# Performance work log

Hardware: AMD Instinct MI355X
Metric: run time of the kernel (lower is better)

Reference implementation:

```python
import jax, jax.numpy as jnp
import numpy as np

EPS_AGG = 1e-6
EPS_BN = 1e-5
EPS_LN = 1e-5


def _bn(t, g, b):
    # BatchNorm1d in training mode: batch statistics over dim 0
    m = t.mean(0)
    v = t.var(0)
    return (t - m) * jax.lax.rsqrt(v + EPS_BN) * g + b


def _gated_gcn(x, e, src, dst, Aw, Ab, Bw, Bb, Cw, Cb, Dw, Db, Ew, Eb, gx, bx, ge, be):
    # GraphGPS GatedGCNLayer (residual=True, dropout=0, no PE)
    N = x.shape[0]
    Ax = x @ Aw + Ab
    Bx = x @ Bw + Bb
    Ce = e @ Cw + Cb
    Dx = x @ Dw + Db
    Ex = x @ Ew + Eb
    e_new = Dx[dst] + Ex[src] + Ce            # [E, D] edge gates (i=target, j=source)
    sig = jax.nn.sigmoid(e_new)
    num = jax.ops.segment_sum(sig * Bx[src], dst, num_segments=N)
    den = jax.ops.segment_sum(sig, dst, num_segments=N) + EPS_AGG
    x_new = Ax + num / den
    x = x + jax.nn.relu(_bn(x_new, gx, bx))   # BN -> ReLU -> residual
    e = e + jax.nn.relu(_bn(e_new, ge, be))
    return x, e


def setup_inputs() -> dict:
    key = jax.random.key(0)
    G, NPG, DEG, D = 256, 32, 8, 70
    NC, H = 10, 256
    N, E = G * NPG, G * NPG * DEG
    ks = list(jax.random.split(key, 24))

    def nrm(k, shape):
        return jax.random.normal(k, shape, jnp.float32)

    def lin(k, i, o):
        return nrm(k, (i, o)) / np.float32(np.sqrt(i)), jnp.zeros((o,), jnp.float32)

    x = nrm(ks[0], (N, 1))
    edge_attr = nrm(ks[1], (E, 1))
    base = jnp.repeat(jnp.arange(G, dtype=jnp.int32) * NPG, NPG * DEG)
    src = base + jax.random.randint(ks[2], (E,), 0, NPG, dtype=jnp.int32)
    dst = base + jax.random.randint(ks[3], (E,), 0, NPG, dtype=jnp.int32)
    edge_index = jnp.stack([src, dst])
    batch_index = jnp.repeat(jnp.arange(G, dtype=jnp.int32), NPG)

    inp = {"x": x, "edge_index": edge_index, "edge_attr": edge_attr, "batch_index": batch_index}
    inp["w_node"], inp["b_node"] = lin(ks[4], 1, D)
    inp["w_edge"], inp["b_edge"] = lin(ks[5], 1, D)
    i = 6
    for l in ("1", "2"):
        for nm in ("A", "B", "C", "D", "E"):
            inp[nm + l + "w"], inp[nm + l + "b"] = lin(ks[i], D, D)
            i += 1
        inp["gx" + l], inp["bx" + l] = jnp.ones((D,), jnp.float32), jnp.zeros((D,), jnp.float32)
        inp["ge" + l], inp["be" + l] = jnp.ones((D,), jnp.float32), jnp.zeros((D,), jnp.float32)
    inp["cls1_w"], inp["cls1_b"] = lin(ks[i], 2 * D, H)
    i += 1
    inp["ln_g"], inp["ln_b"] = jnp.ones((H,), jnp.float32), jnp.zeros((H,), jnp.float32)
    inp["cls2_w"], inp["cls2_b"] = lin(ks[i], H, NC)
    return inp


def reference(x, edge_index, edge_attr, batch_index,
              w_node, b_node, w_edge, b_edge,
              A1w, A1b, B1w, B1b, C1w, C1b, D1w, D1b, E1w, E1b, gx1, bx1, ge1, be1,
              A2w, A2b, B2w, B2b, C2w, C2b, D2w, D2b, E2w, E2b, gx2, bx2, ge2, be2,
              cls1_w, cls1_b, ln_g, ln_b, cls2_w, cls2_b):
    src, dst = edge_index[0], edge_index[1]
    bi = np.asarray(batch_index)
    n_iters = int(np.bincount(bi).max() // 2)   # int(max(sizes)/2)
    B = int(bi.max()) + 1

    h = x @ w_node + b_node
    e = edge_attr @ w_edge + b_edge
    h, e = _gated_gcn(h, e, src, dst, A1w, A1b, B1w, B1b, C1w, C1b, D1w, D1b, E1w, E1b, gx1, bx1, ge1, be1)
    for _ in range(n_iters):  # shared conv2 weights
        h, e = _gated_gcn(h, e, src, dst, A2w, A2b, B2w, B2b, C2w, C2b, D2w, D2b, E2w, E2b, gx2, bx2, ge2, be2)

    gmp = jax.ops.segment_max(h, batch_index, num_segments=B)
    cnt = jax.ops.segment_sum(jnp.ones((h.shape[0], 1), h.dtype), batch_index, num_segments=B)
    gap = jax.ops.segment_sum(h, batch_index, num_segments=B) / cnt
    g = jnp.concatenate([gmp, gap], axis=1)            # [B, 2*D]
    g = jax.nn.relu(g @ cls1_w + cls1_b)               # [B, 256]
    mu = g.mean(-1, keepdims=True)
    var = g.var(-1, keepdims=True)
    g = (g - mu) * jax.lax.rsqrt(var + EPS_LN) * ln_g + ln_b
    return g @ cls2_w + cls2_b                         # [B, num_classes]
```

## Files before the change

kernel.cpp:

```cpp
#include <hip/hip_runtime.h>
#include <hip/hip_fp16.h>
#include <math.h>


#define TPB 768
#define NBLK 256
#define DD 70
#define ETS 256
#define NBS 84
#define WTS 80
#define NLAYERS 17
#define SPL 280
#define NSLOT 8
#define EPS_AGG 1e-6f
#define EPS_BN 1e-5f
#define EPS_LN 1e-5f

#define SCX 0
#define SHX 72
#define SCE 144
#define SHE 216
#define SBO 288
#define STATL_F 576

#define OFF_ET   0
#define OFF_HN   (OFF_ET + 72*ETS)
#define OFF_AX   (OFF_HN + 32*NBS)
#define OFF_BX   (OFF_AX + 32*NBS)
#define OFF_DX   (OFF_BX + 32*NBS)
#define OFF_EX   (OFF_DX + 32*NBS)
#define OFF_PAD  (OFF_EX + 32*NBS)
#define OFF_STATL (OFF_PAD + 3584)
#define SMEM_FLOATS (OFF_STATL + STATL_F)
#define SMEM_BYTES  (SMEM_FLOATS*4 + (32+33)*4 + 512 + 512 + 16)

#define EIX(k,e) (((k)<<8) + ((e) ^ ((((k)>>2)&7)<<2)))
#define SIX(j,c) (((j)<<7) + ((c) ^ ((j)&30)))

#define WS_STATS 4096
#define WS_WT    163840

struct GPSParams {
  const float* __restrict__ x; const int* __restrict__ ei; const float* __restrict__ ea;
  const float* __restrict__ wn; const float* __restrict__ bnn;
  const float* __restrict__ we; const float* __restrict__ web;
  const float* __restrict__ Aw[2]; const float* __restrict__ Ab[2];
  const float* __restrict__ Bw[2]; const float* __restrict__ Bb[2];
  const float* __restrict__ Cw[2]; const float* __restrict__ Cb[2];
  const float* __restrict__ Dw[2]; const float* __restrict__ Db[2];
  const float* __restrict__ Ew[2]; const float* __restrict__ Eb[2];
  const float* __restrict__ gx[2]; const float* __restrict__ bx[2];
  const float* __restrict__ ge[2]; const float* __restrict__ gbe[2];
  const float* __restrict__ c1w; const float* __restrict__ c1b;
  const float* __restrict__ lng; const float* __restrict__ lnb;
  const float* __restrict__ c2w; const float* __restrict__ c2b;
  float* __restrict__ out; float* __restrict__ stats; float* __restrict__ wt;
  unsigned* __restrict__ bar;
};

__device__ __forceinline__ void grid_sync(unsigned* b) {
  __syncthreads();
  if (threadIdx.x == 0) {
    unsigned g = __hip_atomic_load(b, __ATOMIC_RELAXED, __HIP_MEMORY_SCOPE_AGENT);
    int leaf = (int)(blockIdx.x >> 4);
    unsigned a = __hip_atomic_fetch_add(b + 32 + leaf*32, 1u, __ATOMIC_ACQ_REL, __HIP_MEMORY_SCOPE_AGENT);
    bool done = false;
    if (a == 15u) {
      unsigned r = __hip_atomic_fetch_add(b + 16, 1u, __ATOMIC_ACQ_REL, __HIP_MEMORY_SCOPE_AGENT);
      if (r == 15u) {
        #pragma unroll
        for (int i2 = 0; i2 < 16; ++i2)
          __hip_atomic_store(b + 32 + i2*32, 0u, __ATOMIC_RELAXED, __HIP_MEMORY_SCOPE_AGENT);
        __hip_atomic_store(b + 16, 0u, __ATOMIC_RELAXED, __HIP_MEMORY_SCOPE_AGENT);
        __hip_atomic_store(b, g + 1u, __ATOMIC_RELEASE, __HIP_MEMORY_SCOPE_AGENT);
        done = true;
      }
    }
    if (!done) {
      while (__hip_atomic_load(b, __ATOMIC_ACQUIRE, __HIP_MEMORY_SCOPE_AGENT) == g)
        __builtin_amdgcn_s_sleep(2);
    }
  }
  __syncthreads();
}

__global__ void __launch_bounds__(TPB)
__attribute__((amdgpu_waves_per_eu(3, 3)))
gps_kernel(GPSParams p) {
  extern __shared__ float smem[];
  float* eT    = smem + OFF_ET;
  float* hN    = smem + OFF_HN;
  float* Ax    = smem + OFF_AX;
  float* Bx    = smem + OFF_BX;
  float* Dx    = smem + OFF_DX;
  float* Ex    = smem + OFF_EX;
  float* statl = smem + OFF_STATL;
  unsigned* sigb = (unsigned*)(smem + OFF_DX);
  const __half* sigh = (const __half*)sigb;
  int*   icur  = (int*)(smem + SMEM_FLOATS);
  int*   ioff  = icur + 32;
  unsigned char* srcloc = (unsigned char*)(ioff + 33);
  unsigned char* dstloc = srcloc + 256;
  unsigned short* eidxS = (unsigned short*)(dstloc + 256);

  const int tid  = threadIdx.x;
  const int g    = blockIdx.x;
  const int lane = tid & 63;
  const int wid  = tid >> 6;

  const int jbe = wid * 6;
  const int e0  = lane * 4;
  const int n_m  = wid & 3;
  const int n_jb = (wid >> 2) * 24 + (lane >> 3) * 3;
  const int n_n0 = (lane & 7) * 4;

  float* slot = p.stats + ((g & 7) * NLAYERS) * SPL;

  if (tid < 32) icur[tid] = 0;
  __syncthreads();
  if (tid < 256) {
    int s0 = p.ei[g*256 + tid]         - g*32;
    int d0 = p.ei[65536 + g*256 + tid] - g*32;
    srcloc[tid] = (unsigned char)s0;
    dstloc[tid] = (unsigned char)d0;
    atomicAdd(&icur[d0], 1);
  }
  __syncthreads();
  if (tid == 0) {
    int o = 0;
    for (int n = 0; n < 32; ++n) { ioff[n] = o; o += icur[n]; }
    ioff[32] = o;
  }
  __syncthreads();
  if (tid < 32) icur[tid] = ioff[tid];
  __syncthreads();
  if (tid < 256) {
    int d0 = dstloc[tid];
    int sl2 = atomicAdd(&icur[d0], 1);
    eidxS[sl2] = (unsigned short)(tid | ((int)srcloc[tid] << 8));
  }

  for (int i = tid; i < SMEM_FLOATS - OFF_HN; i += TPB) smem[OFF_HN + i] = 0.f;
  for (int i = tid; i < 2*ETS; i += TPB) eT[70*ETS + i] = 0.f;
  __syncthreads();
  for (int i = tid; i < 32*DD; i += TPB) {
    int n = i / DD, j = i % DD;
    hN[n*NBS + j] = fmaf(p.x[g*32 + n], p.wn[j], p.bnn[j]);
  }
  for (int i = tid; i < DD*256; i += TPB) {
    int k = i >> 8, e = i & 255;
    eT[EIX(k, e)] = fmaf(p.ea[g*256 + e], p.we[k], p.web[k]);
  }

  if (g < 10) {
    int ss = g / 5, mm = g % 5;
    const float* W = (mm==0) ? p.Aw[ss] : (mm==1) ? p.Bw[ss] : (mm==2) ? p.Cw[ss]
                   : (mm==3) ? p.Dw[ss] : p.Ew[ss];
    float* dst = p.wt + g * (72*WTS);
    for (int i = tid; i < 72*WTS; i += TPB) {
      int j = i / WTS, k = i - j*WTS;
      dst[i] = (j < DD && k < DD) ? W[k*DD + j] : 0.f;
    }
  }
  grid_sync(p.bar);

  #pragma unroll 1
  for (int L = 0; L < NLAYERS; ++L) {
    const int s = (L == 0) ? 0 : 1;
    float* lslot = slot + L * SPL;
    const float* wbase = p.wt + (size_t)(s*5) * (72*WTS);

    if (tid < DD) statl[SBO + tid] = p.Cb[s][tid] + p.Db[s][tid] + p.Eb[s][tid];

    {
      const float* Wm = wbase + ((n_m==0) ? 0 : (n_m==1) ? 1 : (n_m==2) ? 3 : 4) * (72*WTS);
      float* nbuf = (n_m==0) ? Ax : (n_m==1) ? Bx : (n_m==2) ? Dx : Ex;
      const float* nbias = (n_m==1) ? p.Bb[s] : p.Ab[s];
      float acc[3][4];
      #pragma unroll
      for (int i = 0; i < 3; ++i)
        #pragma unroll
        for (int n = 0; n < 4; ++n) acc[i][n] = 0.f;
      const float* hr0 = hN + n_n0*NBS;
      #pragma unroll 2
      for (int c = 0; c < 18; ++c) {
        const int k0 = c*4;
        float4 h0 = *(const float4*)(hr0 + 0*NBS + k0);
        float4 h1 = *(const float4*)(hr0 + 1*NBS + k0);
        float4 h2 = *(const float4*)(hr0 + 2*NBS + k0);
        float4 h3 = *(const float4*)(hr0 + 3*NBS + k0);
        #pragma unroll
        for (int i = 0; i < 3; ++i) {
          float4 w4 = *(const float4*)(Wm + (n_jb + i)*WTS + k0);
          acc[i][0] = fmaf(h0.x, w4.x, acc[i][0]); acc[i][0] = fmaf(h0.y, w4.y, acc[i][0]);
          acc[i][0] = fmaf(h0.z, w4.z, acc[i][0]); acc[i][0] = fmaf(h0.w, w4.w, acc[i][0]);
          acc[i][1] = fmaf(h1.x, w4.x, acc[i][1]); acc[i][1] = fmaf(h1.y, w4.y, acc[i][1]);
          acc[i][1] = fmaf(h1.z, w4.z, acc[i][1]); acc[i][1] = fmaf(h1.w, w4.w, acc[i][1]);
          acc[i][2] = fmaf(h2.x, w4.x, acc[i][2]); acc[i][2] = fmaf(h2.y, w4.y, acc[i][2]);
          acc[i][2] = fmaf(h2.z, w4.z, acc[i][2]); acc[i][2] = fmaf(h2.w, w4.w, acc[i][2]);
          acc[i][3] = fmaf(h3.x, w4.x, acc[i][3]); acc[i][3] = fmaf(h3.y, w4.y, acc[i][3]);
          acc[i][3] = fmaf(h3.z, w4.z, acc[i][3]); acc[i][3] = fmaf(h3.w, w4.w, acc[i][3]);
        }
      }
      #pragma unroll
      for (int i = 0; i < 3; ++i) {
        int j = n_jb + i;
        if (j < DD) {
          float b = (n_m < 2) ? nbias[j] : 0.f;
          #pragma unroll
          for (int n = 0; n < 4; ++n)
            nbuf[(n_n0 + n)*NBS + j] = acc[i][n] + b;
        }
      }
    }
    __syncthreads();

    const float* wC = wbase + 2 * (72*WTS);
    float eacc[4][6];
    #pragma unroll
    for (int r = 0; r < 4; ++r)
      #pragma unroll
      for (int i = 0; i < 6; ++i) eacc[r][i] = 0.f;

    #pragma unroll 2
    for (int c = 0; c < 18; ++c) {
      const int k0 = c*4;
      float4 ev0 = *(const float4*)(eT + EIX(k0+0, e0));
      float4 ev1 = *(const float4*)(eT + EIX(k0+1, e0));
      float4 ev2 = *(const float4*)(eT + EIX(k0+2, e0));
      float4 ev3 = *(const float4*)(eT + EIX(k0+3, e0));
      #pragma unroll
      for (int i = 0; i < 6; ++i) {
        float4 w4 = *(const float4*)(wC + (jbe + i)*WTS + k0);
        eacc[0][i] = fmaf(ev0.x, w4.x, eacc[0][i]); eacc[1][i] = fmaf(ev0.y, w4.x, eacc[1][i]);
        eacc[2][i] = fmaf(ev0.z, w4.x, eacc[2][i]); eacc[3][i] = fmaf(ev0.w, w4.x, eacc[3][i]);
        eacc[0][i] = fmaf(ev1.x, w4.y, eacc[0][i]); eacc[1][i] = fmaf(ev1.y, w4.y, eacc[1][i]);
        eacc[2][i] = fmaf(ev1.z, w4.y, eacc[2][i]); eacc[3][i] = fmaf(ev1.w, w4.y, eacc[3][i]);
        eacc[0][i] = fmaf(ev2.x, w4.z, eacc[0][i]); eacc[1][i] = fmaf(ev2.y, w4.z, eacc[1][i]);
        eacc[2][i] = fmaf(ev2.z, w4.z, eacc[2][i]); eacc[3][i] = fmaf(ev2.w, w4.z, eacc[3][i]);
        eacc[0][i] = fmaf(ev3.x, w4.w, eacc[0][i]); eacc[1][i] = fmaf(ev3.y, w4.w, eacc[1][i]);
        eacc[2][i] = fmaf(ev3.z, w4.w, eacc[2][i]); eacc[3][i] = fmaf(ev3.w, w4.w, eacc[3][i]);
      }
    }

    {
      int dl0 = dstloc[e0],   sl0 = srcloc[e0];
      int dl1 = dstloc[e0+1], sl1 = srcloc[e0+1];
      int dl2 = dstloc[e0+2], sl2 = srcloc[e0+2];
      int dl3 = dstloc[e0+3], sl3 = srcloc[e0+3];
      #pragma unroll
      for (int i = 0; i < 6; ++i) {
        int j = jbe + i;
        if (j < DD) {
          float bb = statl[SBO + j];
          eacc[0][i] += Dx[dl0*NBS + j] + Ex[sl0*NBS + j] + bb;
          eacc[1][i] += Dx[dl1*NBS + j] + Ex[sl1*NBS + j] + bb;
          eacc[2][i] += Dx[dl2*NBS + j] + Ex[sl2*NBS + j] + bb;
          eacc[3][i] += Dx[dl3*NBS + j] + Ex[sl3*NBS + j] + bb;
        }
      }
    }

    #pragma unroll
    for (int i = 0; i < 6; ++i) {
      int j = jbe + i;
      float ps = (eacc[0][i] + eacc[1][i]) + (eacc[2][i] + eacc[3][i]);
      float qs = eacc[0][i]*eacc[0][i];
      qs = fmaf(eacc[1][i], eacc[1][i], qs);
      qs = fmaf(eacc[2][i], eacc[2][i], qs);
      qs = fmaf(eacc[3][i], eacc[3][i], qs);
      #pragma unroll
      for (int d = 1; d < 64; d <<= 1) {
        ps += __shfl_xor(ps, d, 64);
        qs += __shfl_xor(qs, d, 64);
      }
      if (lane == 0 && j < DD) {
        atomicAdd(lslot + 140 + j, ps);
        atomicAdd(lslot + 210 + j, qs);
      }
    }
    __syncthreads();

    #pragma unroll
    for (int i = 0; i < 6; ++i) {
      int j = jbe + i;
      if (j < DD) {
        float s0 = 1.f / (1.f + __expf(-eacc[0][i]));
        float s1 = 1.f / (1.f + __expf(-eacc[1][i]));
        float s2 = 1.f / (1.f + __expf(-eacc[2][i]));
        float s3 = 1.f / (1.f + __expf(-eacc[3][i]));
        __half2 h01 = __floats2half2_rn(s0, s1);
        __half2 h23 = __floats2half2_rn(s2, s3);
        uint2 pk;
        pk.x = *reinterpret_cast<unsigned*>(&h01);
        pk.y = *reinterpret_cast<unsigned*>(&h23);
        *reinterpret_cast<uint2*>(sigb + SIX(j, 2*lane)) = pk;
      }
    }
    __syncthreads();

    if (tid < 576) {
      int n = tid / 18, jq = tid % 18;
      int j0 = jq * 4;
      bool v2 = (j0 + 2) < DD, v3 = (j0 + 3) < DD;
      float nm0 = 0.f, nm1 = 0.f, nm2 = 0.f, nm3 = 0.f;
      float dn0 = 0.f, dn1 = 0.f, dn2 = 0.f, dn3 = 0.f;
      int pb = ioff[n], pe = ioff[n + 1];
      for (int pp = pb; pp < pe; ++pp) {
        unsigned v = eidxS[pp];
        int e2 = v & 255, sl2 = v >> 8;
        int cb = e2 >> 1, h2 = e2 & 1;
        float s0 = __half2float(sigh[(SIX(j0+0, cb) << 1) + h2]);
        float s1 = __half2float(sigh[(SIX(j0+1, cb) << 1) + h2]);
        float s2 = v2 ? __half2float(sigh[(SIX(j0+2, cb) << 1) + h2]) : 0.f;
        float s3 = v3 ? __half2float(sigh[(SIX(j0+3, cb) << 1) + h2]) : 0.f;
        float4 b4 = *(const float4*)(Bx + sl2*NBS + j0);
        nm0 = fmaf(s0, b4.x, nm0); nm1 = fmaf(s1, b4.y, nm1);
        nm2 = fmaf(s2, b4.z, nm2); nm3 = fmaf(s3, b4.w, nm3);
        dn0 += s0; dn1 += s1; dn2 += s2; dn3 += s3;
      }
      float* axp = Ax + n*NBS + j0;
      float4 ax = *(const float4*)axp;
      ax.x += nm0 / (dn0 + EPS_AGG);
      ax.y += nm1 / (dn1 + EPS_AGG);
      ax.z += nm2 / (dn2 + EPS_AGG);
      ax.w += nm3 / (dn3 + EPS_AGG);
      *(float4*)axp = ax;
    }
    __syncthreads();

    if (tid < SPL) {
      int col = tid % DD, q = tid / DD;
      float sm = 0.f, sq = 0.f;
      #pragma unroll
      for (int r = 0; r < 8; ++r) {
        float v = Ax[(q*8 + r)*NBS + col];
        sm += v; sq = fmaf(v, v, sq);
      }
      atomicAdd(lslot + col, sm);
      atomicAdd(lslot + 70 + col, sq);
    }

    grid_sync(p.bar);

    if (tid < DD) {
      float sm = 0.f, sq = 0.f;
      #pragma unroll
      for (int sl2 = 0; sl2 < NSLOT; ++sl2) {
        const float* st = p.stats + (sl2*NLAYERS + L)*SPL;
        sm += __hip_atomic_load(st + tid,      __ATOMIC_RELAXED, __HIP_MEMORY_SCOPE_AGENT);
        sq += __hip_atomic_load(st + 70 + tid, __ATOMIC_RELAXED, __HIP_MEMORY_SCOPE_AGENT);
      }
      float mean = sm * (1.f/8192.f);
      float var  = sq * (1.f/8192.f) - mean*mean;
      float sc = p.gx[s][tid] * rsqrtf(var + EPS_BN);
      statl[SCX + tid] = sc;
      statl[SHX + tid] = fmaf(-mean, sc, p.bx[s][tid]);
    } else if (tid < 140) {
      int j = tid - DD;
      float sm = 0.f, sq = 0.f;
      #pragma unroll
      for (int sl2 = 0; sl2 < NSLOT; ++sl2) {
        const float* st = p.stats + (sl2*NLAYERS + L)*SPL;
        sm += __hip_atomic_load(st + 140 + j, __ATOMIC_RELAXED, __HIP_MEMORY_SCOPE_AGENT);
        sq += __hip_atomic_load(st + 210 + j, __ATOMIC_RELAXED, __HIP_MEMORY_SCOPE_AGENT);
      }
      float mean = sm * (1.f/65536.f);
      float var  = sq * (1.f/65536.f) - mean*mean;
      float sc = p.ge[s][j] * rsqrtf(var + EPS_BN);
      statl[SCE + j] = sc;
      statl[SHE + j] = fmaf(-mean, sc, p.gbe[s][j]);
    }
    __syncthreads();

    #pragma unroll
    for (int r = 0; r < 3; ++r) {
      int idx = tid + r*TPB;
      int n = idx / 72, j = idx - n*72;
      if (j < DD) {
        float xn = Ax[n*NBS + j];
        hN[n*NBS + j] += fmaxf(fmaf(xn, statl[SCX + j], statl[SHX + j]), 0.f);
      }
    }
    #pragma unroll
    for (int i = 0; i < 6; ++i) {
      int j = jbe + i;
      if (j < DD) {
        float sc = statl[SCE + j], sh = statl[SHE + j];
        float* ep = eT + EIX(j, e0);
        float4 eo = *(const float4*)ep;
        eo.x += fmaxf(fmaf(eacc[0][i], sc, sh), 0.f);
        eo.y += fmaxf(fmaf(eacc[1][i], sc, sh), 0.f);
        eo.z += fmaxf(fmaf(eacc[2][i], sc, sh), 0.f);
        eo.w += fmaxf(fmaf(eacc[3][i], sc, sh), 0.f);
        *(float4*)ep = eo;
      }
    }
    __syncthreads();
  }

  if (tid < DD) {
    float mx = -3.4e38f, sm = 0.f;
    #pragma unroll 4
    for (int r = 0; r < 32; ++r) {
      float v = hN[r*NBS + tid];
      mx = fmaxf(mx, v); sm += v;
    }
    statl[tid]      = mx;
    statl[70 + tid] = sm * (1.f/32.f);
  }
  __syncthreads();
  if (tid < 256) {
    float a = p.c1b[tid];
    for (int k = 0; k < DD; ++k) a = fmaf(statl[k],      p.c1w[k*256 + tid], a);
    for (int k = 0; k < DD; ++k) a = fmaf(statl[70 + k], p.c1w[(DD + k)*256 + tid], a);
    Ax[tid] = fmaxf(a, 0.f);
  }
  __syncthreads();
  if (tid == 0) {
    float sm = 0.f, sq = 0.f;
    for (int k = 0; k < 256; ++k) { float v = Ax[k]; sm += v; sq = fmaf(v, v, sq); }
    float mean = sm * (1.f/256.f);
    float var  = sq * (1.f/256.f) - mean*mean;
    statl[560] = mean;
    statl[561] = rsqrtf(var + EPS_LN);
  }
  __syncthreads();
  if (tid < 256) {
    float v = (Ax[tid] - statl[560]) * statl[561];
    Bx[tid] = fmaf(v, p.lng[tid], p.lnb[tid]);
  }
  __syncthreads();
  if (tid < 10) {
    float a = p.c2b[tid];
    for (int k = 0; k < 256; ++k) a = fmaf(Bx[k], p.c2w[k*10 + tid], a);
    p.out[g*10 + tid] = a;
  }
}

extern "C" void kernel_launch(void* const* d_in, const int* in_sizes, int n_in,
                              void* d_out, int out_size, void* d_ws, size_t ws_size,
                              hipStream_t stream) {
  (void)in_sizes; (void)n_in; (void)out_size; (void)ws_size;
  GPSParams p;
  p.x   = (const float*)d_in[0];
  p.ei  = (const int*)  d_in[1];
  p.ea  = (const float*)d_in[2];
  p.wn  = (const float*)d_in[4];  p.bnn = (const float*)d_in[5];
  p.we  = (const float*)d_in[6];  p.web = (const float*)d_in[7];
  int i = 8;
  for (int s = 0; s < 2; ++s) {
    p.Aw[s] = (const float*)d_in[i++]; p.Ab[s] = (const float*)d_in[i++];
    p.Bw[s] = (const float*)d_in[i++]; p.Bb[s] = (const float*)d_in[i++];
    p.Cw[s] = (const float*)d_in[i++]; p.Cb[s] = (const float*)d_in[i++];
    p.Dw[s] = (const float*)d_in[i++]; p.Db[s] = (const float*)d_in[i++];
    p.Ew[s] = (const float*)d_in[i++]; p.Eb[s] = (const float*)d_in[i++];
    p.gx[s] = (const float*)d_in[i++]; p.bx[s] = (const float*)d_in[i++];
    p.ge[s] = (const float*)d_in[i++]; p.gbe[s] = (const float*)d_in[i++];
  }
  p.c1w = (const float*)d_in[36]; p.c1b = (const float*)d_in[37];
  p.lng = (const float*)d_in[38]; p.lnb = (const float*)d_in[39];
  p.c2w = (const float*)d_in[40]; p.c2b = (const float*)d_in[41];
  p.out = (float*)d_out;
  p.bar = (unsigned*)d_ws;
  p.stats = (float*)((char*)d_ws + WS_STATS);
  p.wt    = (float*)((char*)d_ws + WS_WT);

  hipMemsetAsync(d_ws, 0, WS_STATS + NSLOT*NLAYERS*SPL*4, stream);

  hipFuncSetAttribute((const void*)gps_kernel,
                      hipFuncAttributeMaxDynamicSharedMemorySize, SMEM_BYTES);

  void* args[] = { (void*)&p };
  hipError_t err = hipLaunchCooperativeKernel((const void*)gps_kernel,
                                              dim3(NBLK), dim3(TPB),
                                              args, SMEM_BYTES, stream);
  if (err != hipSuccess) {
    gps_kernel<<<dim3(NBLK), dim3(TPB), SMEM_BYTES, stream>>>(p);
  }
}
```

Measured before the change: 1.068 ms.

## Replace CSR gather aggregation with LDS atomic scatter of sigmoid-weighted messages

Drops the per-block CSR build (counting, prefix scan, bucket fill) and the fp16 sigmoid staging buffer. Each edge thread now computes the sigmoid gates and atomically adds sig*Bx and sig into per-node num/den LDS arrays, and the divide is folded into the BN-stat pass. This removes two block barriers and a separate gather phase, and keeps the gates in fp32 instead of fp16. In exchange it adds many LDS float atomics that collide on the same destination nodes, plus a per-layer zeroing of the accumulators.

```diff
diff --git a/kernel.cpp b/kernel.cpp
--- a/kernel.cpp
+++ b/kernel.cpp
@@ -1,5 +1,4 @@
 #include <hip/hip_runtime.h>
-#include <hip/hip_fp16.h>
 #include <math.h>
 
 
@@ -9,6 +8,7 @@
 #define ETS 256
 #define NBS 84
 #define WTS 80
+#define NDS 73
 #define NLAYERS 17
 #define SPL 280
 #define NSLOT 8
@@ -29,13 +29,13 @@
 #define OFF_BX   (OFF_AX + 32*NBS)
 #define OFF_DX   (OFF_BX + 32*NBS)
 #define OFF_EX   (OFF_DX + 32*NBS)
-#define OFF_PAD  (OFF_EX + 32*NBS)
-#define OFF_STATL (OFF_PAD + 3584)
+#define OFF_NUM  (OFF_EX + 32*NBS)
+#define OFF_DEN  (OFF_NUM + 32*NDS)
+#define OFF_STATL (OFF_DEN + 32*NDS)
 #define SMEM_FLOATS (OFF_STATL + STATL_F)
-#define SMEM_BYTES  (SMEM_FLOATS*4 + (32+33)*4 + 512 + 512 + 16)
+#define SMEM_BYTES  (SMEM_FLOATS*4 + 512 + 16)
 
 #define EIX(k,e) (((k)<<8) + ((e) ^ ((((k)>>2)&7)<<2)))
-#define SIX(j,c) (((j)<<7) + ((c) ^ ((j)&30)))
 
 #define WS_STATS 4096
 #define WS_WT    163840
@@ -94,14 +94,11 @@
   float* Bx    = smem + OFF_BX;
   float* Dx    = smem + OFF_DX;
   float* Ex    = smem + OFF_EX;
+  float* numL  = smem + OFF_NUM;
+  float* denL  = smem + OFF_DEN;
   float* statl = smem + OFF_STATL;
-  unsigned* sigb = (unsigned*)(smem + OFF_DX);
-  const __half* sigh = (const __half*)sigb;
-  int*   icur  = (int*)(smem + SMEM_FLOATS);
-  int*   ioff  = icur + 32;
-  unsigned char* srcloc = (unsigned char*)(ioff + 33);
+  unsigned char* srcloc = (unsigned char*)(smem + SMEM_FLOATS);
   unsigned char* dstloc = srcloc + 256;
-  unsigned short* eidxS = (unsigned short*)(dstloc + 256);
 
   const int tid  = threadIdx.x;
   const int g    = blockIdx.x;
@@ -116,28 +113,9 @@
 
   float* slot = p.stats + ((g & 7) * NLAYERS) * SPL;
 
-  if (tid < 32) icur[tid] = 0;
-  __syncthreads();
   if (tid < 256) {
-    int s0 = p.ei[g*256 + tid]         - g*32;
-    int d0 = p.ei[65536 + g*256 + tid] - g*32;
-    srcloc[tid] = (unsigned char)s0;
-    dstloc[tid] = (unsigned char)d0;
-    atomicAdd(&icur[d0], 1);
-  }
-  __syncthreads();
-  if (tid == 0) {
-    int o = 0;
-    for (int n = 0; n < 32; ++n) { ioff[n] = o; o += icur[n]; }
-    ioff[32] = o;
-  }
-  __syncthreads();
-  if (tid < 32) icur[tid] = ioff[tid];
-  __syncthreads();
-  if (tid < 256) {
-    int d0 = dstloc[tid];
-    int sl2 = atomicAdd(&icur[d0], 1);
-    eidxS[sl2] = (unsigned short)(tid | ((int)srcloc[tid] << 8));
+    srcloc[tid] = (unsigned char)(p.ei[g*256 + tid]         - g*32);
+    dstloc[tid] = (unsigned char)(p.ei[65536 + g*256 + tid] - g*32);
   }
 
   for (int i = tid; i < SMEM_FLOATS - OFF_HN; i += TPB) smem[OFF_HN + i] = 0.f;
@@ -171,6 +149,7 @@
     const float* wbase = p.wt + (size_t)(s*5) * (72*WTS);
 
     if (tid < DD) statl[SBO + tid] = p.Cb[s][tid] + p.Db[s][tid] + p.Eb[s][tid];
+    for (int i = tid; i < 2*32*NDS; i += TPB) numL[i] = 0.f;
 
     {
       const float* Wm = wbase + ((n_m==0) ? 0 : (n_m==1) ? 1 : (n_m==2) ? 3 : 4) * (72*WTS);
@@ -213,7 +192,6 @@
         }
       }
     }
-    __syncthreads();
 
     const float* wC = wbase + 2 * (72*WTS);
     float eacc[4][6];
@@ -242,23 +220,29 @@
         eacc[2][i] = fmaf(ev3.z, w4.w, eacc[2][i]); eacc[3][i] = fmaf(ev3.w, w4.w, eacc[3][i]);
       }
     }
-
-    {
-      int dl0 = dstloc[e0],   sl0 = srcloc[e0];
-      int dl1 = dstloc[e0+1], sl1 = srcloc[e0+1];
-      int dl2 = dstloc[e0+2], sl2 = srcloc[e0+2];
-      int dl3 = dstloc[e0+3], sl3 = srcloc[e0+3];
-      #pragma unroll
-      for (int i = 0; i < 6; ++i) {
-        int j = jbe + i;
-        if (j < DD) {
-          float bb = statl[SBO + j];
-          eacc[0][i] += Dx[dl0*NBS + j] + Ex[sl0*NBS + j] + bb;
-          eacc[1][i] += Dx[dl1*NBS + j] + Ex[sl1*NBS + j] + bb;
-          eacc[2][i] += Dx[dl2*NBS + j] + Ex[sl2*NBS + j] + bb;
-          eacc[3][i] += Dx[dl3*NBS + j] + Ex[sl3*NBS + j] + bb;
-        }
-      }
+    __syncthreads();
+
+    int dl[4], sl[4];
+    #pragma unroll
+    for (int r = 0; r < 4; ++r) { dl[r] = dstloc[e0+r]; sl[r] = srcloc[e0+r]; }
+    float2 bxv[4][3];
+    #pragma unroll
+    for (int r = 0; r < 4; ++r) {
+      const float2* dx2 = (const float2*)(Dx + dl[r]*NBS + jbe);
+      const float2* ex2 = (const float2*)(Ex + sl[r]*NBS + jbe);
+      const float2* bx2 = (const float2*)(Bx + sl[r]*NBS + jbe);
+      float2 d0 = dx2[0], d1 = dx2[1], d2 = dx2[2];
+      float2 x0 = ex2[0], x1 = ex2[1], x2 = ex2[2];
+      bxv[r][0] = bx2[0]; bxv[r][1] = bx2[1]; bxv[r][2] = bx2[2];
+      eacc[r][0] += d0.x + x0.x; eacc[r][1] += d0.y + x0.y;
+      eacc[r][2] += d1.x + x1.x; eacc[r][3] += d1.y + x1.y;
+      eacc[r][4] += d2.x + x2.x; eacc[r][5] += d2.y + x2.y;
+    }
+    #pragma unroll
+    for (int i = 0; i < 6; ++i) {
+      float bb = statl[SBO + jbe + i];
+      #pragma unroll
+      for (int r = 0; r < 4; ++r) eacc[r][i] += bb;
     }
 
     #pragma unroll
@@ -279,53 +263,19 @@
         atomicAdd(lslot + 210 + j, qs);
       }
     }
-    __syncthreads();
 
     #pragma unroll
     for (int i = 0; i < 6; ++i) {
       int j = jbe + i;
       if (j < DD) {
-        float s0 = 1.f / (1.f + __expf(-eacc[0][i]));
-        float s1 = 1.f / (1.f + __expf(-eacc[1][i]));
-        float s2 = 1.f / (1.f + __expf(-eacc[2][i]));
-        float s3 = 1.f / (1.f + __expf(-eacc[3][i]));
-        __half2 h01 = __floats2half2_rn(s0, s1);
-        __half2 h23 = __floats2half2_rn(s2, s3);
-        uint2 pk;
-        pk.x = *reinterpret_cast<unsigned*>(&h01);
-        pk.y = *reinterpret_cast<unsigned*>(&h23);
-        *reinterpret_cast<uint2*>(sigb + SIX(j, 2*lane)) = pk;
-      }
-    }
-    __syncthreads();
-
-    if (tid < 576) {
-      int n = tid / 18, jq = tid % 18;
-      int j0 = jq * 4;
-      bool v2 = (j0 + 2) < DD, v3 = (j0 + 3) < DD;
-      float nm0 = 0.f, nm1 = 0.f, nm2 = 0.f, nm3 = 0.f;
-      float dn0 = 0.f, dn1 = 0.f, dn2 = 0.f, dn3 = 0.f;
-      int pb = ioff[n], pe = ioff[n + 1];
-      for (int pp = pb; pp < pe; ++pp) {
-        unsigned v = eidxS[pp];
-        int e2 = v & 255, sl2 = v >> 8;
-        int cb = e2 >> 1, h2 = e2 & 1;
-        float s0 = __half2float(sigh[(SIX(j0+0, cb) << 1) + h2]);
-        float s1 = __half2float(sigh[(SIX(j0+1, cb) << 1) + h2]);
-        float s2 = v2 ? __half2float(sigh[(SIX(j0+2, cb) << 1) + h2]) : 0.f;
-        float s3 = v3 ? __half2float(sigh[(SIX(j0+3, cb) << 1) + h2]) : 0.f;
-        float4 b4 = *(const float4*)(Bx + sl2*NBS + j0);
-        nm0 = fmaf(s0, b4.x, nm0); nm1 = fmaf(s1, b4.y, nm1);
-        nm2 = fmaf(s2, b4.z, nm2); nm3 = fmaf(s3, b4.w, nm3);
-        dn0 += s0; dn1 += s1; dn2 += s2; dn3 += s3;
-      }
-      float* axp = Ax + n*NBS + j0;
-      float4 ax = *(const float4*)axp;
-      ax.x += nm0 / (dn0 + EPS_AGG);
-      ax.y += nm1 / (dn1 + EPS_AGG);
-      ax.z += nm2 / (dn2 + EPS_AGG);
-      ax.w += nm3 / (dn3 + EPS_AGG);
-      *(float4*)axp = ax;
+        #pragma unroll
+        for (int r = 0; r < 4; ++r) {
+          float sg = 1.f / (1.f + __expf(-eacc[r][i]));
+          float bv = (i & 1) ? bxv[r][i>>1].y : bxv[r][i>>1].x;
+          atomicAdd(&numL[dl[r]*NDS + j], sg * bv);
+          atomicAdd(&denL[dl[r]*NDS + j], sg);
+        }
+      }
     }
     __syncthreads();
 
@@ -334,8 +284,11 @@
       float sm = 0.f, sq = 0.f;
       #pragma unroll
       for (int r = 0; r < 8; ++r) {
-        float v = Ax[(q*8 + r)*NBS + col];
-        sm += v; sq = fmaf(v, v, sq);
+        int n = q*8 + r;
+        float* axp = Ax + n*NBS + col;
+        float x = *axp + numL[n*NDS + col] / (denL[n*NDS + col] + EPS_AGG);
+        *axp = x;
+        sm += x; sq = fmaf(x, x, sq);
       }
       atomicAdd(lslot + col, sm);
       atomicAdd(lslot + 70 + col, sq);
```

After: 1.700 ms. +59.2%, slower.

## Raise block to 1024 threads and re-partition node GEMM, edge GEMM, and gather

Applied to the files above, without the earlier changes.

Raises threads per block from 768 to 1024 and redistributes work. The node GEMM now uses one node per lane with a split-K across half-waves, combined by a shuffle. The edge GEMM gives each thread 2 edges by 9 columns, and the aggregation gather splits each node's edge list between two lanes, combined by a shuffle. Shared memory becomes static and the waves_per_eu attribute is removed. This adds parallelism per CU but raises register pressure and adds shuffle overhead.

```diff
diff --git a/kernel.cpp b/kernel.cpp
--- a/kernel.cpp
+++ b/kernel.cpp
@@ -3,7 +3,7 @@
 #include <math.h>
 
 
-#define TPB 768
+#define TPB 1024
 #define NBLK 256
 #define DD 70
 #define ETS 256
@@ -32,7 +32,6 @@
 #define OFF_PAD  (OFF_EX + 32*NBS)
 #define OFF_STATL (OFF_PAD + 3584)
 #define SMEM_FLOATS (OFF_STATL + STATL_F)
-#define SMEM_BYTES  (SMEM_FLOATS*4 + (32+33)*4 + 512 + 512 + 16)
 
 #define EIX(k,e) (((k)<<8) + ((e) ^ ((((k)>>2)&7)<<2)))
 #define SIX(j,c) (((j)<<7) + ((c) ^ ((j)&30)))
@@ -85,9 +84,14 @@
 }
 
 __global__ void __launch_bounds__(TPB)
-__attribute__((amdgpu_waves_per_eu(3, 3)))
 gps_kernel(GPSParams p) {
-  extern __shared__ float smem[];
+  __shared__ float smem[SMEM_FLOATS];
+  __shared__ int icur[32];
+  __shared__ int ioff[33];
+  __shared__ unsigned char srcloc[256];
+  __shared__ unsigned char dstloc[256];
+  __shared__ unsigned short eidxS[256];
+
   float* eT    = smem + OFF_ET;
   float* hN    = smem + OFF_HN;
   float* Ax    = smem + OFF_AX;
@@ -97,22 +101,20 @@
   float* statl = smem + OFF_STATL;
   unsigned* sigb = (unsigned*)(smem + OFF_DX);
   const __half* sigh = (const __half*)sigb;
-  int*   icur  = (int*)(smem + SMEM_FLOATS);
-  int*   ioff  = icur + 32;
-  unsigned char* srcloc = (unsigned char*)(ioff + 33);
-  unsigned char* dstloc = srcloc + 256;
-  unsigned short* eidxS = (unsigned short*)(dstloc + 256);
 
   const int tid  = threadIdx.x;
   const int g    = blockIdx.x;
   const int lane = tid & 63;
   const int wid  = tid >> 6;
 
-  const int jbe = wid * 6;
-  const int e0  = lane * 4;
+  const int e_cg = wid & 7;
+  const int jbe  = e_cg * 9;
+  const int e0   = (((wid >> 3) << 6) | lane) << 1;
   const int n_m  = wid & 3;
-  const int n_jb = (wid >> 2) * 24 + (lane >> 3) * 3;
-  const int n_n0 = (lane & 7) * 4;
+  const int n_jb = (wid >> 2) * 18;
+  const int n_kh = lane >> 5;
+  const int n_n  = lane & 31;
+  const int n_k0 = n_kh * 40;
 
   float* slot = p.stats + ((g & 7) * NLAYERS) * SPL;
 
@@ -176,99 +178,88 @@
       const float* Wm = wbase + ((n_m==0) ? 0 : (n_m==1) ? 1 : (n_m==2) ? 3 : 4) * (72*WTS);
       float* nbuf = (n_m==0) ? Ax : (n_m==1) ? Bx : (n_m==2) ? Dx : Ex;
       const float* nbias = (n_m==1) ? p.Bb[s] : p.Ab[s];
-      float acc[3][4];
-      #pragma unroll
-      for (int i = 0; i < 3; ++i)
+      float acc[18];
+      #pragma unroll
+      for (int i = 0; i < 18; ++i) acc[i] = 0.f;
+      const float* hrow = hN + n_n*NBS + n_k0;
+      #pragma unroll 1
+      for (int c = 0; c < 5; ++c) {
+        float4 ha = *(const float4*)(hrow + c*8);
+        float4 hb = *(const float4*)(hrow + c*8 + 4);
         #pragma unroll
-        for (int n = 0; n < 4; ++n) acc[i][n] = 0.f;
-      const float* hr0 = hN + n_n0*NBS;
-      #pragma unroll 2
-      for (int c = 0; c < 18; ++c) {
-        const int k0 = c*4;
-        float4 h0 = *(const float4*)(hr0 + 0*NBS + k0);
-        float4 h1 = *(const float4*)(hr0 + 1*NBS + k0);
-        float4 h2 = *(const float4*)(hr0 + 2*NBS + k0);
-        float4 h3 = *(const float4*)(hr0 + 3*NBS + k0);
+        for (int i = 0; i < 18; ++i) {
+          const float* wr = Wm + (n_jb + i)*WTS + n_k0 + c*8;
+          float4 wa = *(const float4*)(wr);
+          float4 wb = *(const float4*)(wr + 4);
+          acc[i] = fmaf(ha.x, wa.x, acc[i]); acc[i] = fmaf(ha.y, wa.y, acc[i]);
+          acc[i] = fmaf(ha.z, wa.z, acc[i]); acc[i] = fmaf(ha.w, wa.w, acc[i]);
+          acc[i] = fmaf(hb.x, wb.x, acc[i]); acc[i] = fmaf(hb.y, wb.y, acc[i]);
+          acc[i] = fmaf(hb.z, wb.z, acc[i]); acc[i] = fmaf(hb.w, wb.w, acc[i]);
+        }
+      }
+      #pragma unroll
+      for (int i = 0; i < 18; ++i) acc[i] += __shfl_xor(acc[i], 32, 64);
+      if (n_kh == 0) {
         #pragma unroll
-        for (int i = 0; i < 3; ++i) {
-          float4 w4 = *(const float4*)(Wm + (n_jb + i)*WTS + k0);
-          acc[i][0] = fmaf(h0.x, w4.x, acc[i][0]); acc[i][0] = fmaf(h0.y, w4.y, acc[i][0]);
-          acc[i][0] = fmaf(h0.z, w4.z, acc[i][0]); acc[i][0] = fmaf(h0.w, w4.w, acc[i][0]);
-          acc[i][1] = fmaf(h1.x, w4.x, acc[i][1]); acc[i][1] = fmaf(h1.y, w4.y, acc[i][1]);
-          acc[i][1] = fmaf(h1.z, w4.z, acc[i][1]); acc[i][1] = fmaf(h1.w, w4.w, acc[i][1]);
-          acc[i][2] = fmaf(h2.x, w4.x, acc[i][2]); acc[i][2] = fmaf(h2.y, w4.y, acc[i][2]);
-          acc[i][2] = fmaf(h2.z, w4.z, acc[i][2]); acc[i][2] = fmaf(h2.w, w4.w, acc[i][2]);
-          acc[i][3] = fmaf(h3.x, w4.x, acc[i][3]); acc[i][3] = fmaf(h3.y, w4.y, acc[i][3]);
-          acc[i][3] = fmaf(h3.z, w4.z, acc[i][3]); acc[i][3] = fmaf(h3.w, w4.w, acc[i][3]);
+        for (int i = 0; i < 18; ++i) {
+          int j = n_jb + i;
+          if (j < DD) {
+            float b = (n_m < 2) ? nbias[j] : 0.f;
+            nbuf[n_n*NBS + j] = acc[i] + b;
+          }
         }
       }
-      #pragma unroll
-      for (int i = 0; i < 3; ++i) {
-        int j = n_jb + i;
-        if (j < DD) {
-          float b = (n_m < 2) ? nbias[j] : 0.f;
-          #pragma unroll
-          for (int n = 0; n < 4; ++n)
-            nbuf[(n_n0 + n)*NBS + j] = acc[i][n] + b;
-        }
-      }
-    }
-    __syncthreads();
+    }
 
     const float* wC = wbase + 2 * (72*WTS);
-    float eacc[4][6];
+    float eacc[2][9];
     #pragma unroll
-    for (int r = 0; r < 4; ++r)
-      #pragma unroll
-      for (int i = 0; i < 6; ++i) eacc[r][i] = 0.f;
-
-    #pragma unroll 2
-    for (int c = 0; c < 18; ++c) {
-      const int k0 = c*4;
-      float4 ev0 = *(const float4*)(eT + EIX(k0+0, e0));
-      float4 ev1 = *(const float4*)(eT + EIX(k0+1, e0));
-      float4 ev2 = *(const float4*)(eT + EIX(k0+2, e0));
-      float4 ev3 = *(const float4*)(eT + EIX(k0+3, e0));
-      #pragma unroll
-      for (int i = 0; i < 6; ++i) {
-        float4 w4 = *(const float4*)(wC + (jbe + i)*WTS + k0);
-        eacc[0][i] = fmaf(ev0.x, w4.x, eacc[0][i]); eacc[1][i] = fmaf(ev0.y, w4.x, eacc[1][i]);
-        eacc[2][i] = fmaf(ev0.z, w4.x, eacc[2][i]); eacc[3][i] = fmaf(ev0.w, w4.x, eacc[3][i]);
-        eacc[0][i] = fmaf(ev1.x, w4.y, eacc[0][i]); eacc[1][i] = fmaf(ev1.y, w4.y, eacc[1][i]);
-        eacc[2][i] = fmaf(ev1.z, w4.y, eacc[2][i]); eacc[3][i] = fmaf(ev1.w, w4.y, eacc[3][i]);
-        eacc[0][i] = fmaf(ev2.x, w4.z, eacc[0][i]); eacc[1][i] = fmaf(ev2.y, w4.z, eacc[1][i]);
-        eacc[2][i] = fmaf(ev2.z, w4.z, eacc[2][i]); eacc[3][i] = fmaf(ev2.w, w4.z, eacc[3][i]);
-        eacc[0][i] = fmaf(ev3.x, w4.w, eacc[0][i]); eacc[1][i] = fmaf(ev3.y, w4.w, eacc[1][i]);
-        eacc[2][i] = fmaf(ev3.z, w4.w, eacc[2][i]); eacc[3][i] = fmaf(ev3.w, w4.w, eacc[3][i]);
-      }
-    }
+    for (int r = 0; r < 2; ++r)
+      #pragma unroll
+      for (int i = 0; i < 9; ++i) eacc[r][i] = 0.f;
+
+    #pragma unroll 1
+    for (int c = 0; c < 9; ++c) {
+      const int k0 = c*8;
+      float2 ev[8];
+      #pragma unroll
+      for (int kk = 0; kk < 8; ++kk)
+        ev[kk] = *(const float2*)(eT + EIX(k0 + kk, e0));
+      #pragma unroll
+      for (int i = 0; i < 9; ++i) {
+        const float* wr = wC + (jbe + i)*WTS + k0;
+        float4 wa = *(const float4*)(wr);
+        float4 wb = *(const float4*)(wr + 4);
+        eacc[0][i] = fmaf(ev[0].x, wa.x, eacc[0][i]); eacc[1][i] = fmaf(ev[0].y, wa.x, eacc[1][i]);
+        eacc[0][i] = fmaf(ev[1].x, wa.y, eacc[0][i]); eacc[1][i] = fmaf(ev[1].y, wa.y, eacc[1][i]);
+        eacc[0][i] = fmaf(ev[2].x, wa.z, eacc[0][i]); eacc[1][i] = fmaf(ev[2].y, wa.z, eacc[1][i]);
+        eacc[0][i] = fmaf(ev[3].x, wa.w, eacc[0][i]); eacc[1][i] = fmaf(ev[3].y, wa.w, eacc[1][i]);
+        eacc[0][i] = fmaf(ev[4].x, wb.x, eacc[0][i]); eacc[1][i] = fmaf(ev[4].y, wb.x, eacc[1][i]);
+        eacc[0][i] = fmaf(ev[5].x, wb.y, eacc[0][i]); eacc[1][i] = fmaf(ev[5].y, wb.y, eacc[1][i]);
+        eacc[0][i] = fmaf(ev[6].x, wb.z, eacc[0][i]); eacc[1][i] = fmaf(ev[6].y, wb.z, eacc[1][i]);
+        eacc[0][i] = fmaf(ev[7].x, wb.w, eacc[0][i]); eacc[1][i] = fmaf(ev[7].y, wb.w, eacc[1][i]);
+      }
+    }
+    __syncthreads();
 
     {
       int dl0 = dstloc[e0],   sl0 = srcloc[e0];
       int dl1 = dstloc[e0+1], sl1 = srcloc[e0+1];
-      int dl2 = dstloc[e0+2], sl2 = srcloc[e0+2];
-      int dl3 = dstloc[e0+3], sl3 = srcloc[e0+3];
-      #pragma unroll
-      for (int i = 0; i < 6; ++i) {
+      const float* dx0 = Dx + dl0*NBS; const float* ex0 = Ex + sl0*NBS;
+      const float* dx1 = Dx + dl1*NBS; const float* ex1 = Ex + sl1*NBS;
+      #pragma unroll
+      for (int i = 0; i < 9; ++i) {
         int j = jbe + i;
-        if (j < DD) {
-          float bb = statl[SBO + j];
-          eacc[0][i] += Dx[dl0*NBS + j] + Ex[sl0*NBS + j] + bb;
-          eacc[1][i] += Dx[dl1*NBS + j] + Ex[sl1*NBS + j] + bb;
-          eacc[2][i] += Dx[dl2*NBS + j] + Ex[sl2*NBS + j] + bb;
-          eacc[3][i] += Dx[dl3*NBS + j] + Ex[sl3*NBS + j] + bb;
-        }
-      }
-    }
-
+        float bb = statl[SBO + j];
+        eacc[0][i] += dx0[j] + ex0[j] + bb;
+        eacc[1][i] += dx1[j] + ex1[j] + bb;
+      }
+    }
     #pragma unroll
-    for (int i = 0; i < 6; ++i) {
+    for (int i = 0; i < 9; ++i) {
       int j = jbe + i;
-      float ps = (eacc[0][i] + eacc[1][i]) + (eacc[2][i] + eacc[3][i]);
-      float qs = eacc[0][i]*eacc[0][i];
-      qs = fmaf(eacc[1][i], eacc[1][i], qs);
-      qs = fmaf(eacc[2][i], eacc[2][i], qs);
-      qs = fmaf(eacc[3][i], eacc[3][i], qs);
+      float ps = eacc[0][i] + eacc[1][i];
+      float qs = fmaf(eacc[0][i], eacc[0][i], eacc[1][i]*eacc[1][i]);
       #pragma unroll
       for (int d = 1; d < 64; d <<= 1) {
         ps += __shfl_xor(ps, d, 64);
@@ -282,50 +273,57 @@
     __syncthreads();
 
     #pragma unroll
-    for (int i = 0; i < 6; ++i) {
+    for (int i = 0; i < 9; ++i) {
       int j = jbe + i;
       if (j < DD) {
         float s0 = 1.f / (1.f + __expf(-eacc[0][i]));
         float s1 = 1.f / (1.f + __expf(-eacc[1][i]));
-        float s2 = 1.f / (1.f + __expf(-eacc[2][i]));
-        float s3 = 1.f / (1.f + __expf(-eacc[3][i]));
         __half2 h01 = __floats2half2_rn(s0, s1);
-        __half2 h23 = __floats2half2_rn(s2, s3);
-        uint2 pk;
-        pk.x = *reinterpret_cast<unsigned*>(&h01);
-        pk.y = *reinterpret_cast<unsigned*>(&h23);
-        *reinterpret_cast<uint2*>(sigb + SIX(j, 2*lane)) = pk;
-      }
-    }
-    __syncthreads();
-
-    if (tid < 576) {
-      int n = tid / 18, jq = tid % 18;
-      int j0 = jq * 4;
-      bool v2 = (j0 + 2) < DD, v3 = (j0 + 3) < DD;
-      float nm0 = 0.f, nm1 = 0.f, nm2 = 0.f, nm3 = 0.f;
-      float dn0 = 0.f, dn1 = 0.f, dn2 = 0.f, dn3 = 0.f;
-      int pb = ioff[n], pe = ioff[n + 1];
-      for (int pp = pb; pp < pe; ++pp) {
-        unsigned v = eidxS[pp];
-        int e2 = v & 255, sl2 = v >> 8;
-        int cb = e2 >> 1, h2 = e2 & 1;
-        float s0 = __half2float(sigh[(SIX(j0+0, cb) << 1) + h2]);
-        float s1 = __half2float(sigh[(SIX(j0+1, cb) << 1) + h2]);
-        float s2 = v2 ? __half2float(sigh[(SIX(j0+2, cb) << 1) + h2]) : 0.f;
-        float s3 = v3 ? __half2float(sigh[(SIX(j0+3, cb) << 1) + h2]) : 0.f;
-        float4 b4 = *(const float4*)(Bx + sl2*NBS + j0);
-        nm0 = fmaf(s0, b4.x, nm0); nm1 = fmaf(s1, b4.y, nm1);
-        nm2 = fmaf(s2, b4.z, nm2); nm3 = fmaf(s3, b4.w, nm3);
-        dn0 += s0; dn1 += s1; dn2 += s2; dn3 += s3;
-      }
-      float* axp = Ax + n*NBS + j0;
-      float4 ax = *(const float4*)axp;
-      ax.x += nm0 / (dn0 + EPS_AGG);
-      ax.y += nm1 / (dn1 + EPS_AGG);
-      ax.z += nm2 / (dn2 + EPS_AGG);
-      ax.w += nm3 / (dn3 + EPS_AGG);
-      *(float4*)axp = ax;
+        sigb[SIX(j, e0 >> 1)] = *reinterpret_cast<unsigned*>(&h01);
+      }
+    }
+    __syncthreads();
+
+    {
+      auto gath = [&](int item, int sub) {
+        int n = item / 18, jq = item % 18;
+        int j0 = jq * 4;
+        bool v2 = (j0 + 2) < DD, v3 = (j0 + 3) < DD;
+        float nm0 = 0.f, nm1 = 0.f, nm2 = 0.f, nm3 = 0.f;
+        float dn0 = 0.f, dn1 = 0.f, dn2 = 0.f, dn3 = 0.f;
+        int pb = ioff[n], pe = ioff[n + 1];
+        int mid = (pb + pe + 1) >> 1;
+        int lo = sub ? mid : pb;
+        int hi = sub ? pe : mid;
+        for (int pp = lo; pp < hi; ++pp) {
+          unsigned v = eidxS[pp];
+          int e2 = v & 255, sl2 = v >> 8;
+          int cb = e2 >> 1, h2 = e2 & 1;
+          float s0 = __half2float(sigh[(SIX(j0+0, cb) << 1) + h2]);
+          float s1 = __half2float(sigh[(SIX(j0+1, cb) << 1) + h2]);
+          float s2 = v2 ? __half2float(sigh[(SIX(j0+2, cb) << 1) + h2]) : 0.f;
+          float s3 = v3 ? __half2float(sigh[(SIX(j0+3, cb) << 1) + h2]) : 0.f;
+          float4 b4 = *(const float4*)(Bx + sl2*NBS + j0);
+          nm0 = fmaf(s0, b4.x, nm0); nm1 = fmaf(s1, b4.y, nm1);
+          nm2 = fmaf(s2, b4.z, nm2); nm3 = fmaf(s3, b4.w, nm3);
+          dn0 += s0; dn1 += s1; dn2 += s2; dn3 += s3;
+        }
+        nm0 += __shfl_xor(nm0, 1, 64); dn0 += __shfl_xor(dn0, 1, 64);
+        nm1 += __shfl_xor(nm1, 1, 64); dn1 += __shfl_xor(dn1, 1, 64);
+        nm2 += __shfl_xor(nm2, 1, 64); dn2 += __shfl_xor(dn2, 1, 64);
+        nm3 += __shfl_xor(nm3, 1, 64); dn3 += __shfl_xor(dn3, 1, 64);
+        if (sub == 0) {
+          float* axp = Ax + n*NBS + j0;
+          float4 ax = *(const float4*)axp;
+          ax.x += nm0 / (dn0 + EPS_AGG);
+          ax.y += nm1 / (dn1 + EPS_AGG);
+          ax.z += nm2 / (dn2 + EPS_AGG);
+          ax.w += nm3 / (dn3 + EPS_AGG);
+          *(float4*)axp = ax;
+        }
+      };
+      gath(tid >> 1, tid & 1);
+      if (tid < 128) gath(512 + (tid >> 1), tid & 1);
     }
     __syncthreads();
 
@@ -376,24 +374,24 @@
     #pragma unroll
     for (int r = 0; r < 3; ++r) {
       int idx = tid + r*TPB;
-      int n = idx / 72, j = idx - n*72;
-      if (j < DD) {
-        float xn = Ax[n*NBS + j];
-        hN[n*NBS + j] += fmaxf(fmaf(xn, statl[SCX + j], statl[SHX + j]), 0.f);
+      if (idx < 2304) {
+        int n = idx / 72, j = idx - n*72;
+        if (j < DD) {
+          float xn = Ax[n*NBS + j];
+          hN[n*NBS + j] += fmaxf(fmaf(xn, statl[SCX + j], statl[SHX + j]), 0.f);
+        }
       }
     }
     #pragma unroll
-    for (int i = 0; i < 6; ++i) {
+    for (int i = 0; i < 9; ++i) {
       int j = jbe + i;
       if (j < DD) {
         float sc = statl[SCE + j], sh = statl[SHE + j];
         float* ep = eT + EIX(j, e0);
-        float4 eo = *(const float4*)ep;
+        float2 eo = *(const float2*)ep;
         eo.x += fmaxf(fmaf(eacc[0][i], sc, sh), 0.f);
         eo.y += fmaxf(fmaf(eacc[1][i], sc, sh), 0.f);
-        eo.z += fmaxf(fmaf(eacc[2][i], sc, sh), 0.f);
-        eo.w += fmaxf(fmaf(eacc[3][i], sc, sh), 0.f);
-        *(float4*)ep = eo;
+        *(float2*)ep = eo;
       }
     }
     __syncthreads();
@@ -468,14 +466,11 @@
 
   hipMemsetAsync(d_ws, 0, WS_STATS + NSLOT*NLAYERS*SPL*4, stream);
 
-  hipFuncSetAttribute((const void*)gps_kernel,
-                      hipFuncAttributeMaxDynamicSharedMemorySize, SMEM_BYTES);
-
   void* args[] = { (void*)&p };
   hipError_t err = hipLaunchCooperativeKernel((const void*)gps_kernel,
                                               dim3(NBLK), dim3(TPB),
-                                              args, SMEM_BYTES, stream);
+                                              args, 0, stream);
   if (err != hipSuccess) {
-    gps_kernel<<<dim3(NBLK), dim3(TPB), SMEM_BYTES, stream>>>(p);
+    gps_kernel<<<dim3(NBLK), dim3(TPB), 0, stream>>>(p);
   }
 }
```

Measured after the change: 2.045 ms. 91.5% more time.

## Store edge sigmoids edge-major and vectorize gather reads, moving a barrier later

Applied to the files above, without the earlier changes.

The half-precision sigmoid buffer changes from a feature-major swizzled layout to an edge-major layout with row stride 36 words. The aggregation loop can then fetch four gates with one 64-bit LDS read instead of four scalar half reads. The Dx/Ex gather in the edge update becomes float2 vector loads, and the barrier before the Ce GEMM moves after it so that GEMM overlaps with stragglers from the node GEMM. The reordered barrier and the larger sigmoid region (256×36 words overlapping Dx/Ex/pad) carry correctness risk, and the edge-major writes may cause bank conflicts.

```diff
diff --git a/kernel.cpp b/kernel.cpp
--- a/kernel.cpp
+++ b/kernel.cpp
@@ -9,6 +9,7 @@
 #define ETS 256
 #define NBS 84
 #define WTS 80
+#define SGS 36
 #define NLAYERS 17
 #define SPL 280
 #define NSLOT 8
@@ -30,12 +31,11 @@
 #define OFF_DX   (OFF_BX + 32*NBS)
 #define OFF_EX   (OFF_DX + 32*NBS)
 #define OFF_PAD  (OFF_EX + 32*NBS)
-#define OFF_STATL (OFF_PAD + 3584)
+#define OFF_STATL (OFF_DX + 256*SGS)
 #define SMEM_FLOATS (OFF_STATL + STATL_F)
-#define SMEM_BYTES  (SMEM_FLOATS*4 + (32+33)*4 + 512 + 512 + 16)
+#define SMEM_BYTES  (SMEM_FLOATS*4 + 2048)
 
 #define EIX(k,e) (((k)<<8) + ((e) ^ ((((k)>>2)&7)<<2)))
-#define SIX(j,c) (((j)<<7) + ((c) ^ ((j)&30)))
 
 #define WS_STATS 4096
 #define WS_WT    163840
@@ -96,7 +96,6 @@
   float* Ex    = smem + OFF_EX;
   float* statl = smem + OFF_STATL;
   unsigned* sigb = (unsigned*)(smem + OFF_DX);
-  const __half* sigh = (const __half*)sigb;
   int*   icur  = (int*)(smem + SMEM_FLOATS);
   int*   ioff  = icur + 32;
   unsigned char* srcloc = (unsigned char*)(ioff + 33);
@@ -213,7 +212,6 @@
         }
       }
     }
-    __syncthreads();
 
     const float* wC = wbase + 2 * (72*WTS);
     float eacc[4][6];
@@ -242,25 +240,29 @@
         eacc[2][i] = fmaf(ev3.z, w4.w, eacc[2][i]); eacc[3][i] = fmaf(ev3.w, w4.w, eacc[3][i]);
       }
     }
+    __syncthreads();
 
     {
-      int dl0 = dstloc[e0],   sl0 = srcloc[e0];
-      int dl1 = dstloc[e0+1], sl1 = srcloc[e0+1];
-      int dl2 = dstloc[e0+2], sl2 = srcloc[e0+2];
-      int dl3 = dstloc[e0+3], sl3 = srcloc[e0+3];
+      int dl[4], sl[4];
+      #pragma unroll
+      for (int r = 0; r < 4; ++r) { dl[r] = dstloc[e0+r]; sl[r] = srcloc[e0+r]; }
+      #pragma unroll
+      for (int r = 0; r < 4; ++r) {
+        const float2* dx2 = (const float2*)(Dx + dl[r]*NBS + jbe);
+        const float2* ex2 = (const float2*)(Ex + sl[r]*NBS + jbe);
+        float2 d0 = dx2[0], d1 = dx2[1], d2 = dx2[2];
+        float2 x0 = ex2[0], x1 = ex2[1], x2 = ex2[2];
+        eacc[r][0] += d0.x + x0.x; eacc[r][1] += d0.y + x0.y;
+        eacc[r][2] += d1.x + x1.x; eacc[r][3] += d1.y + x1.y;
+        eacc[r][4] += d2.x + x2.x; eacc[r][5] += d2.y + x2.y;
+      }
       #pragma unroll
       for (int i = 0; i < 6; ++i) {
-        int j = jbe + i;
-        if (j < DD) {
-          float bb = statl[SBO + j];
-          eacc[0][i] += Dx[dl0*NBS + j] + Ex[sl0*NBS + j] + bb;
-          eacc[1][i] += Dx[dl1*NBS + j] + Ex[sl1*NBS + j] + bb;
-          eacc[2][i] += Dx[dl2*NBS + j] + Ex[sl2*NBS + j] + bb;
-          eacc[3][i] += Dx[dl3*NBS + j] + Ex[sl3*NBS + j] + bb;
-        }
-      }
-    }
-
+        float bb = statl[SBO + jbe + i];
+        #pragma unroll
+        for (int r = 0; r < 4; ++r) eacc[r][i] += bb;
+      }
+    }
     #pragma unroll
     for (int i = 0; i < 6; ++i) {
       int j = jbe + i;
@@ -282,19 +284,17 @@
     __syncthreads();
 
     #pragma unroll
-    for (int i = 0; i < 6; ++i) {
-      int j = jbe + i;
-      if (j < DD) {
-        float s0 = 1.f / (1.f + __expf(-eacc[0][i]));
-        float s1 = 1.f / (1.f + __expf(-eacc[1][i]));
-        float s2 = 1.f / (1.f + __expf(-eacc[2][i]));
-        float s3 = 1.f / (1.f + __expf(-eacc[3][i]));
-        __half2 h01 = __floats2half2_rn(s0, s1);
-        __half2 h23 = __floats2half2_rn(s2, s3);
-        uint2 pk;
-        pk.x = *reinterpret_cast<unsigned*>(&h01);
-        pk.y = *reinterpret_cast<unsigned*>(&h23);
-        *reinterpret_cast<uint2*>(sigb + SIX(j, 2*lane)) = pk;
+    for (int r = 0; r < 4; ++r) {
+      unsigned* srow = sigb + (e0 + r)*SGS + (jbe >> 1);
+      #pragma unroll
+      for (int t = 0; t < 3; ++t) {
+        int j = jbe + 2*t;
+        if (j + 1 < DD) {
+          float sa = 1.f / (1.f + __expf(-eacc[r][2*t]));
+          float sb = 1.f / (1.f + __expf(-eacc[r][2*t+1]));
+          __half2 hh = __floats2half2_rn(sa, sb);
+          srow[t] = *reinterpret_cast<unsigned*>(&hh);
+        }
       }
     }
     __syncthreads();
@@ -309,11 +309,14 @@
       for (int pp = pb; pp < pe; ++pp) {
         unsigned v = eidxS[pp];
         int e2 = v & 255, sl2 = v >> 8;
-        int cb = e2 >> 1, h2 = e2 & 1;
-        float s0 = __half2float(sigh[(SIX(j0+0, cb) << 1) + h2]);
-        float s1 = __half2float(sigh[(SIX(j0+1, cb) << 1) + h2]);
-        float s2 = v2 ? __half2float(sigh[(SIX(j0+2, cb) << 1) + h2]) : 0.f;
-        float s3 = v3 ? __half2float(sigh[(SIX(j0+3, cb) << 1) + h2]) : 0.f;
+        uint2 sg2 = *(const uint2*)(sigb + e2*SGS + (j0 >> 1));
+        __half2 p01 = *reinterpret_cast<const __half2*>(&sg2.x);
+        __half2 p23 = *reinterpret_cast<const __half2*>(&sg2.y);
+        float2 f01 = __half22float2(p01);
+        float2 f23 = __half22float2(p23);
+        float s0 = f01.x, s1 = f01.y;
+        float s2 = v2 ? f23.x : 0.f;
+        float s3 = v3 ? f23.y : 0.f;
         float4 b4 = *(const float4*)(Bx + sl2*NBS + j0);
         nm0 = fmaf(s0, b4.x, nm0); nm1 = fmaf(s1, b4.y, nm1);
         nm2 = fmaf(s2, b4.z, nm2); nm3 = fmaf(s3, b4.w, nm3);
```

Result: faster. 909.8 us (-14.8%).
